# Optimization experiments

Measured on AMD Instinct MI355X. Metric: run time of the kernel, lower is better.

## Reference

```python
import jax, jax.numpy as jnp
import numpy as np

H = 1024        # hidden_size
NH = 16         # num heads
HD = H // NH    # head dim = 64
B, S = 2, 2048


def _linear_params(key, fan_in, fan_out):
    k1, k2 = jax.random.split(key)
    bound = 1.0 / np.sqrt(fan_in)
    w = jax.random.uniform(k1, (fan_in, fan_out), jnp.float32, -bound, bound)
    b = jax.random.uniform(k2, (fan_out,), jnp.float32, -bound, bound)
    return w, b


def setup_inputs() -> dict:
    key = jax.random.key(0)
    ks = jax.random.split(key, 10)
    hidden_states = jax.random.normal(ks[0], (B, S, H), jnp.float32)
    topic_states = jax.random.normal(ks[1], (B, H), jnp.float32)
    attention_mask = jnp.zeros((B, 1, 1, S), jnp.float32)
    Wq, bq = _linear_params(ks[2], H, H)
    Wk, bk = _linear_params(ks[3], H, H)
    Wv, bv = _linear_params(ks[4], H, H)
    Wtp, btp = _linear_params(ks[5], H, H)
    Wta, bta = _linear_params(ks[6], H, H)
    Wd, bd = _linear_params(ks[7], H, H)
    ln_g = jnp.ones((H,), jnp.float32)
    ln_b = jnp.zeros((H,), jnp.float32)
    return {
        "hidden_states": hidden_states, "topic_states": topic_states,
        "attention_mask": attention_mask,
        "Wq": Wq, "bq": bq, "Wk": Wk, "bk": bk, "Wv": Wv, "bv": bv,
        "Wtp": Wtp, "btp": btp, "Wta": Wta, "bta": bta,
        "Wd": Wd, "bd": bd, "ln_g": ln_g, "ln_b": ln_b,
    }


def reference(hidden_states, topic_states, attention_mask,
              Wq, bq, Wk, bk, Wv, bv, Wtp, btp, Wta, bta, Wd, bd, ln_g, ln_b):
    # topic gating: two linears on [B,H], broadcast over seq
    topic_proj = topic_states @ Wtp + btp
    topic_att = topic_proj @ Wta + bta                     # [B,H]
    gate = jax.nn.sigmoid(topic_att)[:, None, :]           # [B,1,H]

    q = hidden_states @ Wq + bq                            # [B,S,H]
    k = (hidden_states @ Wk + bk) * gate                   # sigmoid-gated keys
    v = hidden_states @ Wv + bv

    def split_heads(x):  # [B,S,H] -> [B,NH,S,HD]
        return x.reshape(B, S, NH, HD).transpose(0, 2, 1, 3)

    qh, kh, vh = split_heads(q), split_heads(k), split_heads(v)

    scores = jnp.einsum('bhqd,bhkd->bhqk', qh, kh) / np.sqrt(HD).astype(np.float32)
    scores = scores + attention_mask                       # additive mask
    probs = jax.nn.softmax(scores, axis=-1)                # dropout = identity (eval)
    ctx = jnp.einsum('bhqk,bhkd->bhqd', probs, vh)
    ctx = ctx.transpose(0, 2, 1, 3).reshape(B, S, H)

    out = ctx @ Wd + bd                                    # dense + (eval) dropout
    x = out + hidden_states                                # residual
    mu = jnp.mean(x, axis=-1, keepdims=True)
    var = jnp.mean(jnp.square(x - mu), axis=-1, keepdims=True)
    return (x - mu) * jax.lax.rsqrt(var + 1e-5) * ln_g + ln_b
```

## Files before the change

kernel.cpp:

```cpp
#include <hip/hip_runtime.h>

typedef unsigned short u16;
typedef unsigned int   u32;
typedef __attribute__((ext_vector_type(4)))  float f32x4;
typedef __attribute__((ext_vector_type(16))) float f32x16;
typedef __attribute__((ext_vector_type(8)))  __bf16 bf16x8;
typedef __attribute__((ext_vector_type(8)))  u16  u16x8;
typedef __attribute__((ext_vector_type(4)))  u16  u16x4;

#define HDIM 1024
#define SEQ  2048
#define NB   2
#define MROWS 4096
#define QSCALE 0.18033688011111793f
#define LOG2E  1.4426950408889634f
#define TOPK 64
#define TOPC 16

__device__ __forceinline__ u16 f2bf(float f) {
  u32 u = __float_as_uint(f);
  u32 r = u + 0x7FFFu + ((u >> 16) & 1u);
  return (u16)(r >> 16);
}

__device__ __forceinline__ u32 pkbf(float a, float b) {
  union { __bf16 h[2]; u32 w; } u;
  u.h[0] = (__bf16)a; u.h[1] = (__bf16)b;
  return u.w;
}

__device__ __forceinline__ void gload_lds16(const void* gp, void* lp) {
  __builtin_amdgcn_global_load_lds(
      (const __attribute__((address_space(1))) void*)gp,
      (__attribute__((address_space(3))) void*)lp, 16, 0, 0);
}

__global__ void wt_bf16_kernel(const float* __restrict__ w0, const float* __restrict__ w1,
                               const float* __restrict__ w2, const float* __restrict__ w3,
                               u16* __restrict__ out) {
  const float* W = (blockIdx.z == 0) ? w0 : (blockIdx.z == 1) ? w1 : (blockIdx.z == 2) ? w2 : w3;
  u16* Wt = out + (size_t)blockIdx.z * HDIM * HDIM;
  __shared__ float t[32][33];
  const int k0 = blockIdx.x * 32, n0 = blockIdx.y * 32;
  const int tx = threadIdx.x, ty = threadIdx.y;
#pragma unroll
  for (int j = 0; j < 32; j += 8)
    t[ty + j][tx] = W[(size_t)(k0 + ty + j) * HDIM + n0 + tx];
  __syncthreads();
#pragma unroll
  for (int j = 0; j < 32; j += 8)
    Wt[(size_t)(n0 + ty + j) * HDIM + k0 + tx] = f2bf(t[tx][ty + j]);
}

__global__ void cvt_bf16_kernel(const float* __restrict__ in, u16* __restrict__ out) {
  const size_t i = (size_t)blockIdx.x * 256 + threadIdx.x;
  f32x4 v = *(const f32x4*)(in + i * 4);
  u16x4 o;
#pragma unroll
  for (int e = 0; e < 4; ++e) o[e] = f2bf(v[e]);
  *(u16x4*)(out + i * 4) = o;
}

__global__ void topic_partial_kernel(const float* __restrict__ in, const float* __restrict__ W,
                                     float* __restrict__ part) {
  const int c = blockIdx.x;
  const int b = blockIdx.y;
  const int t = threadIdx.x;
  const float* inb = in + b * HDIM + c * TOPK;
  f32x4 acc = {};
#pragma unroll 8
  for (int k = 0; k < TOPK; ++k) {
    const f32x4 w4 = *(const f32x4*)(W + (size_t)(c * TOPK + k) * HDIM + t * 4);
    acc += inb[k] * w4;
  }
  *(f32x4*)(part + ((size_t)(b * TOPC + c)) * HDIM + t * 4) = acc;
}

__global__ void topic_reduce_kernel(const float* __restrict__ part, const float* __restrict__ bias,
                                    float* __restrict__ out, int sigmoid_mode) {
  const int b = blockIdx.y;
  const int n = blockIdx.x * 256 + threadIdx.x;
  float s = bias[n];
#pragma unroll
  for (int c = 0; c < TOPC; ++c) s += part[((size_t)(b * TOPC + c)) * HDIM + n];
  out[b * HDIM + n] = sigmoid_mode ? (1.f / (1.f + __expf(-s))) : s;
}

template <int MODE>
__global__ __launch_bounds__(256, 2)
void gemm_kernel(const u16* __restrict__ A, const u16* __restrict__ Wt,
                 const float* __restrict__ b0, const float* __restrict__ b1,
                 const float* __restrict__ b2, const float* __restrict__ gate,
                 const float* __restrict__ resid,
                 u16* __restrict__ outb, u16* __restrict__ outv, float* __restrict__ outf) {
  const int n0 = blockIdx.x * 128;
  const int m0 = blockIdx.y * 128;
  const int z = blockIdx.z;
  const u16* W = Wt + (size_t)z * (HDIM * HDIM);
  const float* bias = (MODE == 0) ? (z == 0 ? b0 : (z == 1 ? b1 : b2)) : b0;

  __shared__ __align__(16) u16 Alds[128 * 64];
  __shared__ __align__(16) u16 Blds[128 * 64];

  const int tid = threadIdx.x;
  const int lane = tid & 63;
  const int w = tid >> 6;
  const int wm = w >> 1, wn = w & 1;
  const int srow = tid >> 3, sslot = tid & 7;

  f32x4 acc[4][4] = {};

  for (int k0 = 0; k0 < HDIM; k0 += 64) {
    __syncthreads();
#pragma unroll
    for (int j = 0; j < 4; ++j) {
      const int row = j * 32 + srow;
      const int gs = (sslot ^ (row & 7)) * 8;
      gload_lds16(A + (size_t)(m0 + row) * HDIM + k0 + gs, Alds + j * 2048 + w * 512);
      gload_lds16(W + (size_t)(n0 + row) * HDIM + k0 + gs, Blds + j * 2048 + w * 512);
    }
    __syncthreads();
#pragma unroll
    for (int kk = 0; kk < 2; ++kk) {
      const int slot = ((((kk << 2) + (lane >> 4)) ^ (lane & 7)) << 3);
      bf16x8 af[4], bfr[4];
#pragma unroll
      for (int i = 0; i < 4; ++i) {
        af[i]  = *(const bf16x8*)(&Alds[(wm * 64 + i * 16 + (lane & 15)) * 64 + slot]);
        bfr[i] = *(const bf16x8*)(&Blds[(wn * 64 + i * 16 + (lane & 15)) * 64 + slot]);
      }
#pragma unroll
      for (int i = 0; i < 4; ++i)
#pragma unroll
        for (int jn = 0; jn < 4; ++jn)
          acc[i][jn] = __builtin_amdgcn_mfma_f32_16x16x32_bf16(af[i], bfr[jn], acc[i][jn], 0, 0, 0);
    }
  }

  const int rbase = (lane >> 4) << 2;
  if (MODE == 0 && z == 2) {
#pragma unroll
    for (int i = 0; i < 4; ++i) {
#pragma unroll
      for (int jn = 0; jn < 4; ++jn) {
        const int n = n0 + wn * 64 + jn * 16 + (lane & 15);
        const float bv = bias[n];
        const int m = m0 + wm * 64 + i * 16 + rbase;
        u16x4 o;
#pragma unroll
        for (int r = 0; r < 4; ++r) o[r] = f2bf(acc[i][jn][r] + bv);
        *(u16x4*)(outv + ((size_t)((m >> 11) * 16 + (n >> 6)) * 64 + (n & 63)) * SEQ + (m & 2047)) = o;
      }
    }
    return;
  }
#pragma unroll
  for (int i = 0; i < 4; ++i) {
#pragma unroll
    for (int jn = 0; jn < 4; ++jn) {
      const int n = n0 + wn * 64 + jn * 16 + (lane & 15);
      const float bv = bias[n];
#pragma unroll
      for (int r = 0; r < 4; ++r) {
        const int m = m0 + wm * 64 + i * 16 + rbase + r;
        float v = acc[i][jn][r] + bv;
        if (MODE == 0) {
          if (z == 0) v *= QSCALE;
          if (z == 1) v *= gate[(m >> 11) * HDIM + n];
          outb[(size_t)z * MROWS * HDIM + (size_t)m * HDIM + n] = f2bf(v);
        } else {
          v += resid[(size_t)m * HDIM + n];
          outf[(size_t)m * HDIM + n] = v;
        }
      }
    }
  }
}

__global__ __launch_bounds__(256, 2)
void attn_kernel(const u16* __restrict__ Q, const u16* __restrict__ K,
                 const u16* __restrict__ Vt, const float* __restrict__ mask,
                 u16* __restrict__ O) {
  const int q0 = blockIdx.x * 128;
  const int h = blockIdx.y;
  const int b = blockIdx.z;
  const size_t base = ((size_t)b * SEQ) * HDIM + h * 64;
  const size_t vtbase = (size_t)((b * 16 + h) * 64) * SEQ;
  const int tid = threadIdx.x, lane = tid & 63, w = tid >> 6;
  const int hh = lane >> 5;
  const int ql = lane & 31;
  const int NT = SEQ / 64;

  __shared__ __align__(16) u16 Kss[2][64 * 64];
  __shared__ __align__(16) u16 Vts[2][64 * 64];

  bf16x8 Qf[4];
  {
    const u16* qp = Q + base + (size_t)(q0 + w * 32 + ql) * HDIM;
#pragma unroll
    for (int ds = 0; ds < 4; ++ds)
      Qf[ds] = *(const bf16x8*)(qp + ds * 16 + hh * 8);
  }

  const int l3 = lane >> 3, l7 = lane & 7;
  const u16* ksrc0 = K + base + (size_t)(w * 8 + l3) * HDIM + ((l7 ^ l3) << 3);
  const u16* ksrc1 = K + base + (size_t)((4 + w) * 8 + l3) * HDIM + ((l7 ^ l3) << 3);
  const u16* vsrc0 = Vt + vtbase + (size_t)(w * 16 + l3) * SEQ + (((l7 ^ l3 ^ (w * 2)) & 7) << 3);
  const u16* vsrc1 = Vt + vtbase + (size_t)(w * 16 + 8 + l3) * SEQ + (((l7 ^ l3 ^ (w * 2 + 1)) & 7) << 3);

  const u16* kaddr[4];
#pragma unroll
  for (int ds = 0; ds < 4; ++ds)
    kaddr[ds] = &Kss[0][ql * 64 + (((ds * 2 + hh) ^ (ql & 7)) << 3)];
  const u16* vaddr[2][4];
#pragma unroll
  for (int dt = 0; dt < 2; ++dt) {
    const int d = dt * 32 + ql;
    const int sw = (d & 7) ^ ((d >> 3) & 7);
#pragma unroll
    for (int c = 0; c < 4; ++c)
      vaddr[dt][c] = &Vts[0][d * 64 + (((c * 2 + hh) ^ sw) << 3)];
  }

  const float* mrow_base = mask + (size_t)b * SEQ + hh * 4;

  float m_run = -1e30f, l_run = 0.f;
  f32x16 accA = {}, accB = {};
  bf16x8 pfA[4], pfB[4];

  auto STAGEK = [&](const int buf, const int t1) {
    const size_t ko = (size_t)(t1 * 64) * HDIM;
    gload_lds16(ksrc0 + ko, &Kss[buf][w * 512]);
    gload_lds16(ksrc1 + ko, &Kss[buf][(4 + w) * 512]);
  };
  auto STAGEV = [&](const int buf, const int t1) {
    const int vo = t1 * 64;
    gload_lds16(vsrc0 + vo, &Vts[buf][w * 1024]);
    gload_lds16(vsrc1 + vo, &Vts[buf][w * 1024 + 512]);
  };

  auto EXPPACK = [&](const f32x16& s0_, const f32x16& s1_, bf16x8 (&pfout)[4]) {
    f32x16 p0_, p1_;
#pragma unroll
    for (int j = 0; j < 16; ++j) {
      p0_[j] = __builtin_amdgcn_exp2f(s0_[j] - m_run);
      p1_[j] = __builtin_amdgcn_exp2f(s1_[j] - m_run);
    }
    float r8[8];
#pragma unroll
    for (int j = 0; j < 8; ++j)
      r8[j] = (p0_[j] + p0_[j + 8]) + (p1_[j] + p1_[j + 8]);
    float rs = ((r8[0] + r8[1]) + (r8[2] + r8[3])) + ((r8[4] + r8[5]) + (r8[6] + r8[7]));
    rs += __shfl_xor(rs, 32);
    l_run += rs;
#pragma unroll
    for (int kvb = 0; kvb < 2; ++kvb) {
      const f32x16& pp = kvb ? p1_ : p0_;
#pragma unroll
      for (int s2 = 0; s2 < 2; ++s2) {
        const u32 a0 = pkbf(pp[s2 * 8 + 0], pp[s2 * 8 + 1]);
        const u32 a1 = pkbf(pp[s2 * 8 + 2], pp[s2 * 8 + 3]);
        const u32 b0v = pkbf(pp[s2 * 8 + 4], pp[s2 * 8 + 5]);
        const u32 b1v = pkbf(pp[s2 * 8 + 6], pp[s2 * 8 + 7]);
        const u32 sd0 = hh ? a0 : b0v, sd1 = hh ? a1 : b1v;
        const u32 r0 = (u32)__shfl_xor((int)sd0, 32);
        const u32 r1 = (u32)__shfl_xor((int)sd1, 32);
        union { u32 u[4]; bf16x8 v; } pu;
        pu.u[0] = hh ? r0 : a0;  pu.u[1] = hh ? r1 : a1;
        pu.u[2] = hh ? b0v : r0; pu.u[3] = hh ? b1v : r1;
        pfout[kvb * 2 + s2] = pu.v;
      }
    }
  };

  auto RESCALE = [&](const float mx) {
    const float mnew = fmaxf(m_run, mx);
    const float corr = __builtin_amdgcn_exp2f(m_run - mnew);
    m_run = mnew; l_run *= corr;
#pragma unroll
    for (int j = 0; j < 16; ++j) {
      const float cj = __shfl(corr, (j & 3) + 8 * (j >> 2) + 4 * hh);
      accA[j] *= cj; accB[j] *= cj;
    }
  };

  auto QKMM = [&](const int tq, const int kb, f32x16& s0_, f32x16& s1_, float& mx) {
    f32x16 sv0 = {}, sv1 = {};
#pragma unroll
    for (int ds = 0; ds < 4; ++ds) {
      const bf16x8 kf0 = *(const bf16x8*)(kaddr[ds] + kb * 4096);
      const bf16x8 kf1 = *(const bf16x8*)(kaddr[ds] + kb * 4096 + 2048);
      sv0 = __builtin_amdgcn_mfma_f32_32x32x16_bf16(kf0, Qf[ds], sv0, 0, 0, 0);
      sv1 = __builtin_amdgcn_mfma_f32_32x32x16_bf16(kf1, Qf[ds], sv1, 0, 0, 0);
    }
    f32x4 m40[4], m41[4];
    const float* mrow = mrow_base + tq * 64;
#pragma unroll
    for (int g = 0; g < 4; ++g) {
      m40[g] = *(const f32x4*)(mrow + g * 8);
      m41[g] = *(const f32x4*)(mrow + 32 + g * 8);
    }
#pragma unroll
    for (int j = 0; j < 16; ++j) {
      s0_[j] = fmaf(m40[j >> 2][j & 3], LOG2E, sv0[j]);
      s1_[j] = fmaf(m41[j >> 2][j & 3], LOG2E, sv1[j]);
    }
    float t8[8];
#pragma unroll
    for (int j = 0; j < 8; ++j)
      t8[j] = fmaxf(fmaxf(s0_[j], s0_[j + 8]), fmaxf(s1_[j], s1_[j + 8]));
    mx = fmaxf(fmaxf(fmaxf(t8[0], t8[1]), fmaxf(t8[2], t8[3])),
               fmaxf(fmaxf(t8[4], t8[5]), fmaxf(t8[6], t8[7])));
    mx = fmaxf(mx, __shfl_xor(mx, 32));
  };

  STAGEK(0, 0); STAGEV(0, 0);
  __syncthreads();
  STAGEK(1, 1); STAGEV(1, 1);
  {
    f32x16 s0_, s1_; float mx;
    QKMM(0, 0, s0_, s1_, mx);
    if (!__all(mx <= m_run + 8.f)) RESCALE(mx);
    EXPPACK(s0_, s1_, pfA);
  }
  __syncthreads();

  auto STEP = [&](const int t, const int X, const bf16x8 (&pfin)[4], bf16x8 (&pfout)[4]) {
    if (t + 2 < NT) STAGEK(X, t + 2);
    f32x16 s0_, s1_; float mx;
    QKMM(t + 1, X ^ 1, s0_, s1_, mx);
    const bool resc = !__all(mx <= m_run + 8.f);
#pragma unroll
    for (int c = 0; c < 4; ++c) {
      const bf16x8 vf0 = *(const bf16x8*)(vaddr[0][c] + X * 4096);
      const bf16x8 vf1 = *(const bf16x8*)(vaddr[1][c] + X * 4096);
      accA = __builtin_amdgcn_mfma_f32_32x32x16_bf16(pfin[c], vf0, accA, 0, 0, 0);
      accB = __builtin_amdgcn_mfma_f32_32x32x16_bf16(pfin[c], vf1, accB, 0, 0, 0);
    }
    if (resc) RESCALE(mx);
    EXPPACK(s0_, s1_, pfout);
    __syncthreads();
    if (t + 2 < NT) STAGEV(X, t + 2);
  };

  for (int t = 0; t < NT - 2; t += 2) {
    STEP(t, 0, pfA, pfB);
    STEP(t + 1, 1, pfB, pfA);
  }
  STEP(NT - 2, 0, pfA, pfB);

#pragma unroll
  for (int c = 0; c < 4; ++c) {
    const bf16x8 vf0 = *(const bf16x8*)(vaddr[0][c] + 4096);
    const bf16x8 vf1 = *(const bf16x8*)(vaddr[1][c] + 4096);
    accA = __builtin_amdgcn_mfma_f32_32x32x16_bf16(pfB[c], vf0, accA, 0, 0, 0);
    accB = __builtin_amdgcn_mfma_f32_32x32x16_bf16(pfB[c], vf1, accB, 0, 0, 0);
  }

  const float linv = 1.f / l_run;
#pragma unroll
  for (int j = 0; j < 16; ++j) {
    const int rq = (j & 3) + 8 * (j >> 2) + 4 * hh;
    const float lj = __shfl(linv, rq);
    const size_t orow = base + (size_t)(q0 + w * 32 + rq) * HDIM;
    O[orow + ql]      = f2bf(accA[j] * lj);
    O[orow + 32 + ql] = f2bf(accB[j] * lj);
  }
}

__global__ void ln_kernel(const float* __restrict__ x, const float* __restrict__ g,
                          const float* __restrict__ bb, float* __restrict__ out) {
  const int row = blockIdx.x;
  const int tid = threadIdx.x;
  const f32x4 v = *(const f32x4*)(x + (size_t)row * HDIM + tid * 4);
  float s = v[0] + v[1] + v[2] + v[3];
  float s2 = v[0] * v[0] + v[1] * v[1] + v[2] * v[2] + v[3] * v[3];
#pragma unroll
  for (int o = 1; o < 64; o <<= 1) { s += __shfl_xor(s, o); s2 += __shfl_xor(s2, o); }
  __shared__ float rs[4], rs2[4];
  if ((tid & 63) == 0) { rs[tid >> 6] = s; rs2[tid >> 6] = s2; }
  __syncthreads();
  s = rs[0] + rs[1] + rs[2] + rs[3];
  s2 = rs2[0] + rs2[1] + rs2[2] + rs2[3];
  const float mu = s * (1.f / HDIM);
  const float var = s2 * (1.f / HDIM) - mu * mu;
  const float inv = rsqrtf(var + 1e-5f);
  f32x4 o4;
#pragma unroll
  for (int e = 0; e < 4; ++e) {
    const int c = tid * 4 + e;
    o4[e] = (v[e] - mu) * inv * g[c] + bb[c];
  }
  *(f32x4*)(out + (size_t)row * HDIM + tid * 4) = o4;
}

extern "C" void kernel_launch(void* const* d_in, const int* in_sizes, int n_in,
                              void* d_out, int out_size, void* d_ws, size_t ws_size,
                              hipStream_t stream) {
  const float* hidden = (const float*)d_in[0];
  const float* topic  = (const float*)d_in[1];
  const float* mask   = (const float*)d_in[2];
  const float* Wq  = (const float*)d_in[3];  const float* bq  = (const float*)d_in[4];
  const float* Wk  = (const float*)d_in[5];  const float* bk  = (const float*)d_in[6];
  const float* Wv  = (const float*)d_in[7];  const float* bv  = (const float*)d_in[8];
  const float* Wtp = (const float*)d_in[9];  const float* btp = (const float*)d_in[10];
  const float* Wta = (const float*)d_in[11]; const float* bta = (const float*)d_in[12];
  const float* Wd  = (const float*)d_in[13]; const float* bd  = (const float*)d_in[14];
  const float* lng = (const float*)d_in[15]; const float* lnb = (const float*)d_in[16];
  float* out = (float*)d_out;

  char* ws = (char*)d_ws;
  u16* hs_bf  = (u16*)(ws);
  u16* WtAll  = (u16*)(ws + (size_t)(8u << 20));
  u16* qkv    = (u16*)(ws + (size_t)(16u << 20));
  u16* ctx    = (u16*)(ws + (size_t)(40u << 20));
  u16* VtG    = (u16*)(ws + (size_t)(48u << 20));
  float* xbuf = (float*)(ws + (size_t)(16u << 20));
  float* tproj = (float*)(ws + (size_t)(64u << 20));
  float* tgate = (float*)(ws + (size_t)(64u << 20) + 8192);
  float* tpart = (float*)(ws + (size_t)(16u << 20));

  wt_bf16_kernel<<<dim3(32, 32, 4), dim3(32, 8), 0, stream>>>(Wq, Wk, Wv, Wd, WtAll);
  cvt_bf16_kernel<<<4096, 256, 0, stream>>>(hidden, hs_bf);
  topic_partial_kernel<<<dim3(TOPC, NB), 256, 0, stream>>>(topic, Wtp, tpart);
  topic_reduce_kernel<<<dim3(4, NB), 256, 0, stream>>>(tpart, btp, tproj, 0);
  topic_partial_kernel<<<dim3(TOPC, NB), 256, 0, stream>>>(tproj, Wta, tpart);
  topic_reduce_kernel<<<dim3(4, NB), 256, 0, stream>>>(tpart, bta, tgate, 1);
  gemm_kernel<0><<<dim3(8, 32, 3), 256, 0, stream>>>(hs_bf, WtAll, bq, bk, bv, tgate,
                                                     nullptr, qkv, VtG, nullptr);
  attn_kernel<<<dim3(16, 16, NB), 256, 0, stream>>>(qkv, qkv + (size_t)MROWS * HDIM,
                                                    VtG, mask, ctx);
  gemm_kernel<1><<<dim3(8, 32, 1), 256, 0, stream>>>(ctx, WtAll + 3 * (size_t)HDIM * HDIM,
                                                     bd, nullptr, nullptr, nullptr, hidden,
                                                     nullptr, nullptr, xbuf);
  ln_kernel<<<4096, 256, 0, stream>>>(xbuf, lng, lnb, out);
}
```

Before: 156.8 us.

## Fuse prep kernels and double attention KV tile to 128 keys

Merges the weight transpose, hidden-state bf16 conversion and first topic projection into one launch, and folds the topic reduce into the second projection, cutting six small launches down to three. The attention kernel now stages 128-key K/V tiles per pipeline step, which halves the number of barriers and softmax max/rescale checks per block. In exchange LDS use doubles to 64 KB and the launch bound no longer requests two blocks per CU, so occupancy may drop and register pressure rises with eight P fragments per buffer.

```diff
diff --git a/kernel.cpp b/kernel.cpp
--- a/kernel.cpp
+++ b/kernel.cpp
@@ -35,55 +35,79 @@
       (__attribute__((address_space(3))) void*)lp, 16, 0, 0);
 }
 
-__global__ void wt_bf16_kernel(const float* __restrict__ w0, const float* __restrict__ w1,
-                               const float* __restrict__ w2, const float* __restrict__ w3,
-                               u16* __restrict__ out) {
-  const float* W = (blockIdx.z == 0) ? w0 : (blockIdx.z == 1) ? w1 : (blockIdx.z == 2) ? w2 : w3;
-  u16* Wt = out + (size_t)blockIdx.z * HDIM * HDIM;
-  __shared__ float t[32][33];
-  const int k0 = blockIdx.x * 32, n0 = blockIdx.y * 32;
-  const int tx = threadIdx.x, ty = threadIdx.y;
-#pragma unroll
-  for (int j = 0; j < 32; j += 8)
-    t[ty + j][tx] = W[(size_t)(k0 + ty + j) * HDIM + n0 + tx];
+__global__ void prep_kernel(const float* __restrict__ w0, const float* __restrict__ w1,
+                            const float* __restrict__ w2, const float* __restrict__ w3,
+                            u16* __restrict__ wt_out,
+                            const float* __restrict__ hidden, u16* __restrict__ hs_out,
+                            const float* __restrict__ topic, const float* __restrict__ Wtp,
+                            float* __restrict__ part1) {
+  const int bid = blockIdx.x;
+  const int tid = threadIdx.x;
+  if (bid < 4096) {
+    const int z = bid >> 10, ny = (bid >> 5) & 31, kx = bid & 31;
+    const float* W = (z == 0) ? w0 : (z == 1) ? w1 : (z == 2) ? w2 : w3;
+    u16* Wt = wt_out + (size_t)z * HDIM * HDIM;
+    __shared__ float t[32][33];
+    const int k0 = kx * 32, n0 = ny * 32;
+    const int tx = tid & 31, ty = tid >> 5;
+#pragma unroll
+    for (int j = 0; j < 32; j += 8)
+      t[ty + j][tx] = W[(size_t)(k0 + ty + j) * HDIM + n0 + tx];
+    __syncthreads();
+#pragma unroll
+    for (int j = 0; j < 32; j += 8)
+      Wt[(size_t)(n0 + ty + j) * HDIM + k0 + tx] = f2bf(t[tx][ty + j]);
+  } else if (bid < 8192) {
+    const size_t i = (size_t)(bid - 4096) * 256 + tid;
+    f32x4 v = *(const f32x4*)(hidden + i * 4);
+    u16x4 o;
+#pragma unroll
+    for (int e = 0; e < 4; ++e) o[e] = f2bf(v[e]);
+    *(u16x4*)(hs_out + i * 4) = o;
+  } else {
+    const int b3 = bid - 8192;
+    const int c = b3 & 15, b = b3 >> 4;
+    const float* inb = topic + b * HDIM + c * TOPK;
+    f32x4 acc = {};
+#pragma unroll 8
+    for (int k = 0; k < TOPK; ++k) {
+      const f32x4 w4 = *(const f32x4*)(Wtp + (size_t)(c * TOPK + k) * HDIM + tid * 4);
+      acc += inb[k] * w4;
+    }
+    *(f32x4*)(part1 + ((size_t)(b * TOPC + c)) * HDIM + tid * 4) = acc;
+  }
+}
+
+__global__ void topic_rp_kernel(const float* __restrict__ part1, const float* __restrict__ btp,
+                                const float* __restrict__ Wta, float* __restrict__ part2) {
+  const int c = blockIdx.x, b = blockIdx.y;
+  const int t = threadIdx.x;
+  __shared__ float inl[TOPK];
+  if (t < TOPK) {
+    float s = btp[c * TOPK + t];
+#pragma unroll
+    for (int cc = 0; cc < TOPC; ++cc)
+      s += part1[((size_t)(b * TOPC + cc)) * HDIM + c * TOPK + t];
+    inl[t] = s;
+  }
   __syncthreads();
-#pragma unroll
-  for (int j = 0; j < 32; j += 8)
-    Wt[(size_t)(n0 + ty + j) * HDIM + k0 + tx] = f2bf(t[tx][ty + j]);
-}
-
-__global__ void cvt_bf16_kernel(const float* __restrict__ in, u16* __restrict__ out) {
-  const size_t i = (size_t)blockIdx.x * 256 + threadIdx.x;
-  f32x4 v = *(const f32x4*)(in + i * 4);
-  u16x4 o;
-#pragma unroll
-  for (int e = 0; e < 4; ++e) o[e] = f2bf(v[e]);
-  *(u16x4*)(out + i * 4) = o;
-}
-
-__global__ void topic_partial_kernel(const float* __restrict__ in, const float* __restrict__ W,
-                                     float* __restrict__ part) {
-  const int c = blockIdx.x;
-  const int b = blockIdx.y;
-  const int t = threadIdx.x;
-  const float* inb = in + b * HDIM + c * TOPK;
   f32x4 acc = {};
 #pragma unroll 8
   for (int k = 0; k < TOPK; ++k) {
-    const f32x4 w4 = *(const f32x4*)(W + (size_t)(c * TOPK + k) * HDIM + t * 4);
-    acc += inb[k] * w4;
-  }
-  *(f32x4*)(part + ((size_t)(b * TOPC + c)) * HDIM + t * 4) = acc;
+    const f32x4 w4 = *(const f32x4*)(Wta + (size_t)(c * TOPK + k) * HDIM + t * 4);
+    acc += inl[k] * w4;
+  }
+  *(f32x4*)(part2 + ((size_t)(b * TOPC + c)) * HDIM + t * 4) = acc;
 }
 
 __global__ void topic_reduce_kernel(const float* __restrict__ part, const float* __restrict__ bias,
-                                    float* __restrict__ out, int sigmoid_mode) {
+                                    float* __restrict__ out) {
   const int b = blockIdx.y;
   const int n = blockIdx.x * 256 + threadIdx.x;
   float s = bias[n];
 #pragma unroll
   for (int c = 0; c < TOPC; ++c) s += part[((size_t)(b * TOPC + c)) * HDIM + n];
-  out[b * HDIM + n] = sigmoid_mode ? (1.f / (1.f + __expf(-s))) : s;
+  out[b * HDIM + n] = 1.f / (1.f + __expf(-s));
 }
 
 template <int MODE>
@@ -177,7 +201,7 @@
   }
 }
 
-__global__ __launch_bounds__(256, 2)
+__global__ __launch_bounds__(256)
 void attn_kernel(const u16* __restrict__ Q, const u16* __restrict__ K,
                  const u16* __restrict__ Vt, const float* __restrict__ mask,
                  u16* __restrict__ O) {
@@ -189,10 +213,10 @@
   const int tid = threadIdx.x, lane = tid & 63, w = tid >> 6;
   const int hh = lane >> 5;
   const int ql = lane & 31;
-  const int NT = SEQ / 64;
-
-  __shared__ __align__(16) u16 Kss[2][64 * 64];
-  __shared__ __align__(16) u16 Vts[2][64 * 64];
+  const int NS = SEQ / 128;
+
+  __shared__ __align__(16) u16 Kss[2][128 * 64];
+  __shared__ __align__(16) u16 Vts[2][64 * 128];
 
   bf16x8 Qf[4];
   {
@@ -203,10 +227,15 @@
   }
 
   const int l3 = lane >> 3, l7 = lane & 7;
-  const u16* ksrc0 = K + base + (size_t)(w * 8 + l3) * HDIM + ((l7 ^ l3) << 3);
-  const u16* ksrc1 = K + base + (size_t)((4 + w) * 8 + l3) * HDIM + ((l7 ^ l3) << 3);
-  const u16* vsrc0 = Vt + vtbase + (size_t)(w * 16 + l3) * SEQ + (((l7 ^ l3 ^ (w * 2)) & 7) << 3);
-  const u16* vsrc1 = Vt + vtbase + (size_t)(w * 16 + 8 + l3) * SEQ + (((l7 ^ l3 ^ (w * 2 + 1)) & 7) << 3);
+  const u16* ksrc = K + base + (size_t)(w * 8 + l3) * HDIM + ((l7 ^ l3) << 3);
+  const u16* vsrc[4];
+#pragma unroll
+  for (int j = 0; j < 4; ++j) {
+    const int d = w * 16 + j * 4 + (lane >> 4);
+    const int sg = lane & 15;
+    const int sw = (d & 7) ^ ((d >> 3) & 7);
+    vsrc[j] = Vt + vtbase + (size_t)d * SEQ + ((sg >> 3) << 6) + (((sg & 7) ^ sw) << 3);
+  }
 
   const u16* kaddr[4];
 #pragma unroll
@@ -219,27 +248,69 @@
     const int sw = (d & 7) ^ ((d >> 3) & 7);
 #pragma unroll
     for (int c = 0; c < 4; ++c)
-      vaddr[dt][c] = &Vts[0][d * 64 + (((c * 2 + hh) ^ sw) << 3)];
+      vaddr[dt][c] = &Vts[0][d * 128 + (((c * 2 + hh) ^ sw) << 3)];
   }
 
   const float* mrow_base = mask + (size_t)b * SEQ + hh * 4;
 
   float m_run = -1e30f, l_run = 0.f;
   f32x16 accA = {}, accB = {};
-  bf16x8 pfA[4], pfB[4];
-
-  auto STAGEK = [&](const int buf, const int t1) {
-    const size_t ko = (size_t)(t1 * 64) * HDIM;
-    gload_lds16(ksrc0 + ko, &Kss[buf][w * 512]);
-    gload_lds16(ksrc1 + ko, &Kss[buf][(4 + w) * 512]);
-  };
-  auto STAGEV = [&](const int buf, const int t1) {
-    const int vo = t1 * 64;
-    gload_lds16(vsrc0 + vo, &Vts[buf][w * 1024]);
-    gload_lds16(vsrc1 + vo, &Vts[buf][w * 1024 + 512]);
-  };
-
-  auto EXPPACK = [&](const f32x16& s0_, const f32x16& s1_, bf16x8 (&pfout)[4]) {
+  bf16x8 pfA[8], pfB[8];
+
+  auto STAGEK = [&](const int buf, const int T1) {
+    const u16* kp = ksrc + (size_t)(T1 * 128) * HDIM;
+#pragma unroll
+    for (int j = 0; j < 4; ++j)
+      gload_lds16(kp + (size_t)(j * 32) * HDIM, &Kss[buf][j * 2048 + w * 512]);
+  };
+  auto STAGEV = [&](const int buf, const int T1) {
+#pragma unroll
+    for (int j = 0; j < 4; ++j)
+      gload_lds16(vsrc[j] + T1 * 128, &Vts[buf][w * 2048 + j * 512]);
+  };
+
+  auto QKMM = [&](const int Tq, const int s, const int kb,
+                  f32x16& s0_, f32x16& s1_, float& mx) {
+    f32x16 sv0 = {}, sv1 = {};
+#pragma unroll
+    for (int ds = 0; ds < 4; ++ds) {
+      const bf16x8 kf0 = *(const bf16x8*)(kaddr[ds] + kb * 8192 + s * 4096);
+      const bf16x8 kf1 = *(const bf16x8*)(kaddr[ds] + kb * 8192 + s * 4096 + 2048);
+      sv0 = __builtin_amdgcn_mfma_f32_32x32x16_bf16(kf0, Qf[ds], sv0, 0, 0, 0);
+      sv1 = __builtin_amdgcn_mfma_f32_32x32x16_bf16(kf1, Qf[ds], sv1, 0, 0, 0);
+    }
+    f32x4 m40[4], m41[4];
+    const float* mrow = mrow_base + Tq * 128 + s * 64;
+#pragma unroll
+    for (int g = 0; g < 4; ++g) {
+      m40[g] = *(const f32x4*)(mrow + g * 8);
+      m41[g] = *(const f32x4*)(mrow + 32 + g * 8);
+    }
+#pragma unroll
+    for (int j = 0; j < 16; ++j) {
+      s0_[j] = fmaf(m40[j >> 2][j & 3], LOG2E, sv0[j]);
+      s1_[j] = fmaf(m41[j >> 2][j & 3], LOG2E, sv1[j]);
+    }
+    float t8[8];
+#pragma unroll
+    for (int j = 0; j < 8; ++j)
+      t8[j] = fmaxf(fmaxf(s0_[j], s0_[j + 8]), fmaxf(s1_[j], s1_[j + 8]));
+    mx = fmaxf(fmaxf(fmaxf(t8[0], t8[1]), fmaxf(t8[2], t8[3])),
+               fmaxf(fmaxf(t8[4], t8[5]), fmaxf(t8[6], t8[7])));
+  };
+
+  auto RESCALE = [&](const float mx) {
+    const float mnew = fmaxf(m_run, mx);
+    const float corr = __builtin_amdgcn_exp2f(m_run - mnew);
+    m_run = mnew; l_run *= corr;
+#pragma unroll
+    for (int j = 0; j < 16; ++j) {
+      const float cj = __shfl(corr, (j & 3) + 8 * (j >> 2) + 4 * hh);
+      accA[j] *= cj; accB[j] *= cj;
+    }
+  };
+
+  auto EXPPACK = [&](const f32x16& s0_, const f32x16& s1_, float& rs_out, bf16x8* pf4) {
     f32x16 p0_, p1_;
 #pragma unroll
     for (int j = 0; j < 16; ++j) {
@@ -250,9 +321,7 @@
 #pragma unroll
     for (int j = 0; j < 8; ++j)
       r8[j] = (p0_[j] + p0_[j + 8]) + (p1_[j] + p1_[j + 8]);
-    float rs = ((r8[0] + r8[1]) + (r8[2] + r8[3])) + ((r8[4] + r8[5]) + (r8[6] + r8[7]));
-    rs += __shfl_xor(rs, 32);
-    l_run += rs;
+    rs_out = ((r8[0] + r8[1]) + (r8[2] + r8[3])) + ((r8[4] + r8[5]) + (r8[6] + r8[7]));
 #pragma unroll
     for (int kvb = 0; kvb < 2; ++kvb) {
       const f32x16& pp = kvb ? p1_ : p0_;
@@ -268,94 +337,67 @@
         union { u32 u[4]; bf16x8 v; } pu;
         pu.u[0] = hh ? r0 : a0;  pu.u[1] = hh ? r1 : a1;
         pu.u[2] = hh ? b0v : r0; pu.u[3] = hh ? b1v : r1;
-        pfout[kvb * 2 + s2] = pu.v;
+        pf4[kvb * 2 + s2] = pu.v;
       }
     }
   };
 
-  auto RESCALE = [&](const float mx) {
-    const float mnew = fmaxf(m_run, mx);
-    const float corr = __builtin_amdgcn_exp2f(m_run - mnew);
-    m_run = mnew; l_run *= corr;
-#pragma unroll
-    for (int j = 0; j < 16; ++j) {
-      const float cj = __shfl(corr, (j & 3) + 8 * (j >> 2) + 4 * hh);
-      accA[j] *= cj; accB[j] *= cj;
-    }
-  };
-
-  auto QKMM = [&](const int tq, const int kb, f32x16& s0_, f32x16& s1_, float& mx) {
-    f32x16 sv0 = {}, sv1 = {};
-#pragma unroll
-    for (int ds = 0; ds < 4; ++ds) {
-      const bf16x8 kf0 = *(const bf16x8*)(kaddr[ds] + kb * 4096);
-      const bf16x8 kf1 = *(const bf16x8*)(kaddr[ds] + kb * 4096 + 2048);
-      sv0 = __builtin_amdgcn_mfma_f32_32x32x16_bf16(kf0, Qf[ds], sv0, 0, 0, 0);
-      sv1 = __builtin_amdgcn_mfma_f32_32x32x16_bf16(kf1, Qf[ds], sv1, 0, 0, 0);
-    }
-    f32x4 m40[4], m41[4];
-    const float* mrow = mrow_base + tq * 64;
-#pragma unroll
-    for (int g = 0; g < 4; ++g) {
-      m40[g] = *(const f32x4*)(mrow + g * 8);
-      m41[g] = *(const f32x4*)(mrow + 32 + g * 8);
-    }
-#pragma unroll
-    for (int j = 0; j < 16; ++j) {
-      s0_[j] = fmaf(m40[j >> 2][j & 3], LOG2E, sv0[j]);
-      s1_[j] = fmaf(m41[j >> 2][j & 3], LOG2E, sv1[j]);
-    }
-    float t8[8];
-#pragma unroll
-    for (int j = 0; j < 8; ++j)
-      t8[j] = fmaxf(fmaxf(s0_[j], s0_[j + 8]), fmaxf(s1_[j], s1_[j + 8]));
-    mx = fmaxf(fmaxf(fmaxf(t8[0], t8[1]), fmaxf(t8[2], t8[3])),
-               fmaxf(fmaxf(t8[4], t8[5]), fmaxf(t8[6], t8[7])));
-    mx = fmaxf(mx, __shfl_xor(mx, 32));
+  auto PVSUB = [&](const int X, const int s, const bf16x8* pf4) {
+#pragma unroll
+    for (int c = 0; c < 4; ++c) {
+      const bf16x8 vf0 = *(const bf16x8*)(vaddr[0][c] + X * 8192 + s * 64);
+      const bf16x8 vf1 = *(const bf16x8*)(vaddr[1][c] + X * 8192 + s * 64);
+      accA = __builtin_amdgcn_mfma_f32_32x32x16_bf16(pf4[c], vf0, accA, 0, 0, 0);
+      accB = __builtin_amdgcn_mfma_f32_32x32x16_bf16(pf4[c], vf1, accB, 0, 0, 0);
+    }
   };
 
   STAGEK(0, 0); STAGEV(0, 0);
   __syncthreads();
   STAGEK(1, 1); STAGEV(1, 1);
   {
-    f32x16 s0_, s1_; float mx;
-    QKMM(0, 0, s0_, s1_, mx);
+    f32x16 sa0, sa1, sb0, sb1; float mxa, mxb;
+    QKMM(0, 0, 0, sa0, sa1, mxa);
+    QKMM(0, 1, 0, sb0, sb1, mxb);
+    float mx = fmaxf(mxa, mxb);
+    mx = fmaxf(mx, __shfl_xor(mx, 32));
     if (!__all(mx <= m_run + 8.f)) RESCALE(mx);
-    EXPPACK(s0_, s1_, pfA);
+    float ra, rb;
+    EXPPACK(sa0, sa1, ra, &pfA[0]);
+    EXPPACK(sb0, sb1, rb, &pfA[4]);
+    float rs = ra + rb; rs += __shfl_xor(rs, 32);
+    l_run += rs;
   }
   __syncthreads();
 
-  auto STEP = [&](const int t, const int X, const bf16x8 (&pfin)[4], bf16x8 (&pfout)[4]) {
-    if (t + 2 < NT) STAGEK(X, t + 2);
-    f32x16 s0_, s1_; float mx;
-    QKMM(t + 1, X ^ 1, s0_, s1_, mx);
+  auto STEP = [&](const int T, const int X, const bf16x8 (&pfin)[8], bf16x8 (&pfout)[8]) {
+    if (T + 2 < NS) STAGEK(X, T + 2);
+    f32x16 sa0, sa1, sb0, sb1; float mxa, mxb;
+    QKMM(T + 1, 0, X ^ 1, sa0, sa1, mxa);
+    QKMM(T + 1, 1, X ^ 1, sb0, sb1, mxb);
+    float mx = fmaxf(mxa, mxb);
+    mx = fmaxf(mx, __shfl_xor(mx, 32));
     const bool resc = !__all(mx <= m_run + 8.f);
-#pragma unroll
-    for (int c = 0; c < 4; ++c) {
-      const bf16x8 vf0 = *(const bf16x8*)(vaddr[0][c] + X * 4096);
-      const bf16x8 vf1 = *(const bf16x8*)(vaddr[1][c] + X * 4096);
-      accA = __builtin_amdgcn_mfma_f32_32x32x16_bf16(pfin[c], vf0, accA, 0, 0, 0);
-      accB = __builtin_amdgcn_mfma_f32_32x32x16_bf16(pfin[c], vf1, accB, 0, 0, 0);
-    }
+    PVSUB(X, 0, &pfin[0]);
+    PVSUB(X, 1, &pfin[4]);
     if (resc) RESCALE(mx);
-    EXPPACK(s0_, s1_, pfout);
+    float ra, rb;
+    EXPPACK(sa0, sa1, ra, &pfout[0]);
+    EXPPACK(sb0, sb1, rb, &pfout[4]);
+    float rs = ra + rb; rs += __shfl_xor(rs, 32);
+    l_run += rs;
     __syncthreads();
-    if (t + 2 < NT) STAGEV(X, t + 2);
-  };
-
-  for (int t = 0; t < NT - 2; t += 2) {
-    STEP(t, 0, pfA, pfB);
-    STEP(t + 1, 1, pfB, pfA);
-  }
-  STEP(NT - 2, 0, pfA, pfB);
-
-#pragma unroll
-  for (int c = 0; c < 4; ++c) {
-    const bf16x8 vf0 = *(const bf16x8*)(vaddr[0][c] + 4096);
-    const bf16x8 vf1 = *(const bf16x8*)(vaddr[1][c] + 4096);
-    accA = __builtin_amdgcn_mfma_f32_32x32x16_bf16(pfB[c], vf0, accA, 0, 0, 0);
-    accB = __builtin_amdgcn_mfma_f32_32x32x16_bf16(pfB[c], vf1, accB, 0, 0, 0);
-  }
+    if (T + 2 < NS) STAGEV(X, T + 2);
+  };
+
+  for (int T = 0; T < NS - 2; T += 2) {
+    STEP(T, 0, pfA, pfB);
+    STEP(T + 1, 1, pfB, pfA);
+  }
+  STEP(NS - 2, 0, pfA, pfB);
+
+  PVSUB(1, 0, &pfB[0]);
+  PVSUB(1, 1, &pfB[4]);
 
   const float linv = 1.f / l_run;
 #pragma unroll
@@ -416,16 +458,14 @@
   u16* ctx    = (u16*)(ws + (size_t)(40u << 20));
   u16* VtG    = (u16*)(ws + (size_t)(48u << 20));
   float* xbuf = (float*)(ws + (size_t)(16u << 20));
-  float* tproj = (float*)(ws + (size_t)(64u << 20));
-  float* tgate = (float*)(ws + (size_t)(64u << 20) + 8192);
-  float* tpart = (float*)(ws + (size_t)(16u << 20));
-
-  wt_bf16_kernel<<<dim3(32, 32, 4), dim3(32, 8), 0, stream>>>(Wq, Wk, Wv, Wd, WtAll);
-  cvt_bf16_kernel<<<4096, 256, 0, stream>>>(hidden, hs_bf);
-  topic_partial_kernel<<<dim3(TOPC, NB), 256, 0, stream>>>(topic, Wtp, tpart);
-  topic_reduce_kernel<<<dim3(4, NB), 256, 0, stream>>>(tpart, btp, tproj, 0);
-  topic_partial_kernel<<<dim3(TOPC, NB), 256, 0, stream>>>(tproj, Wta, tpart);
-  topic_reduce_kernel<<<dim3(4, NB), 256, 0, stream>>>(tpart, bta, tgate, 1);
+  float* tgate = (float*)(ws + (size_t)(64u << 20));
+  float* tpart1 = (float*)(ws + (size_t)(66u << 20));
+  float* tpart2 = (float*)(ws + (size_t)(67u << 20));
+
+  prep_kernel<<<8224, 256, 0, stream>>>(Wq, Wk, Wv, Wd, WtAll, hidden, hs_bf,
+                                        topic, Wtp, tpart1);
+  topic_rp_kernel<<<dim3(TOPC, NB), 256, 0, stream>>>(tpart1, btp, Wta, tpart2);
+  topic_reduce_kernel<<<dim3(4, NB), 256, 0, stream>>>(tpart2, bta, tgate);
   gemm_kernel<0><<<dim3(8, 32, 3), 256, 0, stream>>>(hs_bf, WtAll, bq, bk, bv, tgate,
                                                      nullptr, qkv, VtG, nullptr);
   attn_kernel<<<dim3(16, 16, NB), 256, 0, stream>>>(qkv, qkv + (size_t)MROWS * HDIM,
```

New measurement: 174.8 us. +11.4%, slower.
